# Optimization experiments

Hardware: AMD Instinct MI355X
Metric: run time of the kernel (lower is better)

## Reference

```python
import jax, jax.numpy as jnp
import numpy as np

SCALE = 64 ** (-0.5)


def setup_inputs() -> dict:
    key = jax.random.key(0)
    ks = jax.random.split(key, 6)
    B, C, D, N = 2, 1024, 64, 128
    w_std = C ** (-0.5)
    return {
        "lidar": jax.random.normal(ks[0], (B, C, D, N), dtype=jnp.float32),
        "cam": jax.random.normal(ks[1], (B, C, D, N), dtype=jnp.float32),
        "Wq": jax.random.normal(ks[2], (C, C), dtype=jnp.float32) * w_std,
        "Wk": jax.random.normal(ks[3], (C, C), dtype=jnp.float32) * w_std,
        "Wv": jax.random.normal(ks[4], (C, C), dtype=jnp.float32) * w_std,
        "Wo": jax.random.normal(ks[5], (C, C), dtype=jnp.float32) * w_std,
    }


def _proj(W, x):
    # 1x1 Conv1d over flattened (D*N) positions == channel matmul, bias=False
    return jnp.einsum('oc,bcdn->bodn', W, x)


def reference(lidar, cam, Wq, Wk, Wv, Wo):
    q = _proj(Wq, lidar)  # [B, C, D, Ni]
    k = _proj(Wk, cam)    # [B, C, D, Nj]
    v = _proj(Wv, cam)    # [B, C, D, Nj]
    # contract over D (head-dim-like axis); scores per (batch, channel)
    dots = jnp.einsum('bhdi,bhdj->bhij', q, k) * SCALE  # [B, C, Ni, Nj]
    att = jax.nn.softmax(dots, axis=-1)
    # einsum 'a b i c,a b j c->a b j i': contract over cam positions
    out = jnp.einsum('bhic,bhjc->bhji', att, v)  # [B, C, D, Ni]
    out = jax.nn.gelu(_proj(Wo, out), approximate=False)
    return out
```

## Files before the change

### kernel.cpp

```cpp
#include <hip/hip_runtime.h>
#include <math.h>

#define CH  1024
#define PPB 8192

typedef __attribute__((ext_vector_type(8))) short short8;
typedef __attribute__((ext_vector_type(4))) float f32x4;

__device__ __forceinline__ ushort f2bf(float x) {
    uint u = __float_as_uint(x);
    return (ushort)((u + 0x7FFFu + ((u >> 16) & 1u)) >> 16);
}
__device__ __forceinline__ float bf2f(ushort u) {
    return __uint_as_float(((uint)u) << 16);
}
__device__ __forceinline__ void gload16(const void* g, const void* l) {
    __builtin_amdgcn_global_load_lds((const __attribute__((address_space(1))) void*)g,
                                     (__attribute__((address_space(3))) void*)l, 16, 0, 0);
}

__global__ __launch_bounds__(256) void prep(const float* __restrict__ lidar,
                                            const float* __restrict__ cam,
                                            const float* __restrict__ Wq,
                                            const float* __restrict__ Wk,
                                            const float* __restrict__ Wv,
                                            const float* __restrict__ Wo,
                                            ushort* __restrict__ wdst,
                                            ushort* __restrict__ lidT,
                                            ushort* __restrict__ camT)
{
    __shared__ float T[64][65];
    const int blk = blockIdx.x;
    const int tid = threadIdx.x;

    if (blk < 2048) {
        const int y = blk >> 9;
        const int x = blk & 511;
        const float* w = (y == 0) ? Wq : (y == 1) ? Wk : (y == 2) ? Wv : Wo;
        ushort* o = wdst + (size_t)y * (1u << 20);
        const int idx = (x * 256 + tid) * 8;
        const float4 v0 = *(const float4*)(w + idx);
        const float4 v1 = *(const float4*)(w + idx + 4);
        ushort4 o0, o1;
        o0.x = f2bf(v0.x); o0.y = f2bf(v0.y); o0.z = f2bf(v0.z); o0.w = f2bf(v0.w);
        o1.x = f2bf(v1.x); o1.y = f2bf(v1.y); o1.z = f2bf(v1.z); o1.w = f2bf(v1.w);
        *(ushort4*)(o + idx)     = o0;
        *(ushort4*)(o + idx + 4) = o1;
        return;
    }

    const int t = blk - 2048;
    const bool isLid = (t < 4096);
    const int tt = isLid ? t : t - 4096;
    const float* in = isLid ? lidar : cam;
    ushort* out = isLid ? lidT : camT;

    const int p0 = (tt & 127) * 64;
    const int c0 = ((tt >> 7) & 15) * 64;
    const int b  = tt >> 11;
    const int rc = tid >> 4;
    const int rp = (tid & 15) * 4;

    #pragma unroll
    for (int pass = 0; pass < 4; ++pass) {
        const int c = pass * 16 + rc;
        const size_t base = ((size_t)(b * CH + c0 + c)) * PPB + p0 + rp;
        const float4 v = *(const float4*)(in + base);
        T[c][rp] = v.x; T[c][rp + 1] = v.y; T[c][rp + 2] = v.z; T[c][rp + 3] = v.w;
    }
    __syncthreads();
    #pragma unroll
    for (int pass = 0; pass < 4; ++pass) {
        const int p = pass * 16 + rc;
        ushort4 o;
        o.x = f2bf(T[rp + 0][p]); o.y = f2bf(T[rp + 1][p]);
        o.z = f2bf(T[rp + 2][p]); o.w = f2bf(T[rp + 3][p]);
        *(ushort4*)(out + ((size_t)(b * PPB + p0 + p)) * CH + c0 + rp) = o;
    }
}

__global__ __launch_bounds__(256) void transpose_ao(const ushort* __restrict__ in_,
                                                    ushort* __restrict__ out)
{
    __shared__ float T[64][65];
    const int p0 = blockIdx.x * 64;
    const int c0 = blockIdx.y * 64;
    const int b  = blockIdx.z;
    const int t  = threadIdx.x;
    const int rc = t >> 4;
    const int rp = (t & 15) * 4;

    #pragma unroll
    for (int pass = 0; pass < 4; ++pass) {
        const int c = pass * 16 + rc;
        const size_t base = ((size_t)(b * CH + c0 + c)) * PPB + p0 + rp;
        const ushort4 v = *(const ushort4*)(in_ + base);
        T[c][rp]     = bf2f(v.x); T[c][rp + 1] = bf2f(v.y);
        T[c][rp + 2] = bf2f(v.z); T[c][rp + 3] = bf2f(v.w);
    }
    __syncthreads();
    #pragma unroll
    for (int pass = 0; pass < 4; ++pass) {
        const int p = pass * 16 + rc;
        const int prow = p * 128 + blockIdx.x;
        ushort4 o;
        o.x = f2bf(T[rp + 0][p]); o.y = f2bf(T[rp + 1][p]);
        o.z = f2bf(T[rp + 2][p]); o.w = f2bf(T[rp + 3][p]);
        *(ushort4*)(out + ((size_t)(b * PPB + prow)) * CH + c0 + rp) = o;
    }
}

template <int IS_WO>
__global__ __launch_bounds__(512, 2) void gemm256(const ushort* __restrict__ W3,
                                                  const ushort* __restrict__ lidT,
                                                  const ushort* __restrict__ camT,
                                                  void* __restrict__ outp)
{
    __shared__ __align__(16) ushort sh[65536];
    char* shb = (char*)sh;

    const int bid = blockIdx.x;
    int g, bm, bn;
    if (IS_WO) {
        const int sid = (bid & 7) * 32 + (bid >> 3);
        g = 3; bm = sid & 3; bn = sid >> 2;
    } else {
        const int sid = (bid & 7) * 96 + (bid >> 3);
        g = sid >> 8; const int r = sid & 255; bm = r & 3; bn = r >> 2;
    }
    const int m0  = bm * 256;
    const int b   = bn >> 5;
    const int nn0 = (bn & 31) * 4;
    const int n0  = bn * 256;
    const ushort* A  = W3 + (size_t)g * (1u << 20);
    const ushort* Bt = (g == 0) ? lidT : camT;
    const bool remap = (!IS_WO) && (g < 2);

    const int tid = threadIdx.x;
    const int w   = tid >> 6;
    const int l   = tid & 63;
    const int wr  = w >> 2;
    const int wc  = w & 3;
    const int hi  = l >> 4;
    const int fr  = l & 15;

    auto stageA = [&](int buf, int kt, int half) {
        const int k0 = kt * 64;
        #pragma unroll
        for (int ld = 0; ld < 2; ++ld) {
            const int c  = w * 2 + ld;
            const int rt = half * 128 + c * 8 + (l >> 3);
            const int kc = ((l & 7) ^ (rt & 7)) << 3;
            gload16(A + (size_t)(m0 + rt) * CH + k0 + kc,
                    &shb[buf * 32768 + half * 16384 + c * 1024]);
        }
    };
    auto stageB = [&](int buf, int kt, int half) {
        const int k0 = kt * 64;
        #pragma unroll
        for (int ld = 0; ld < 2; ++ld) {
            const int c  = w * 2 + ld;
            const int rt = half * 128 + c * 8 + (l >> 3);
            const int kc = ((l & 7) ^ (rt & 7)) << 3;
            size_t brow;
            if (remap) brow = (size_t)b * PPB + (size_t)(rt & 63) * 128 + nn0 + (rt >> 6);
            else       brow = (size_t)(n0 + rt);
            gload16(Bt + brow * CH + k0 + kc,
                    &shb[65536 + buf * 32768 + half * 16384 + c * 1024]);
        }
    };

    f32x4 acc[8][4];
    #pragma unroll
    for (int i = 0; i < 8; ++i)
        #pragma unroll
        for (int j = 0; j < 4; ++j) acc[i][j] = (f32x4)(0.0f);

    stageA(0, 0, 0); stageA(0, 0, 1); stageB(0, 0, 0); stageB(0, 0, 1);

    for (int kt = 0; kt < 16; ++kt) {
        const int buf = kt & 1, nxt = buf ^ 1;
        if (kt < 15) {
            stageA(nxt, kt + 1, 0);
            __builtin_amdgcn_sched_barrier(0);
            asm volatile("s_waitcnt vmcnt(2)" ::: "memory");
        } else {
            __builtin_amdgcn_sched_barrier(0);
            asm volatile("s_waitcnt vmcnt(0)" ::: "memory");
        }
        __builtin_amdgcn_s_barrier();
        __builtin_amdgcn_sched_barrier(0);
        const int Ab = buf * 32768, Bb = 65536 + buf * 32768;

        #pragma unroll
        for (int q = 0; q < 4; ++q) {
            const int mh = q >> 1, nh = q & 1;
            if (kt < 15) {
                if (q == 1) stageA(nxt, kt + 1, 1);
                else if (q == 2) stageB(nxt, kt + 1, 0);
                else if (q == 3) stageB(nxt, kt + 1, 1);
            }
            short8 aq[4][2], bq[2][2];
            #pragma unroll
            for (int fm = 0; fm < 4; ++fm) {
                const int row = wr * 128 + (mh * 4 + fm) * 16 + fr;
                #pragma unroll
                for (int kk = 0; kk < 2; ++kk)
                    aq[fm][kk] = *(const short8*)&shb[Ab + row * 128 +
                        ((((kk << 2) + hi) ^ (row & 7)) << 4)];
            }
            #pragma unroll
            for (int fn = 0; fn < 2; ++fn) {
                const int row = wc * 64 + (nh * 2 + fn) * 16 + fr;
                #pragma unroll
                for (int kk = 0; kk < 2; ++kk)
                    bq[fn][kk] = *(const short8*)&shb[Bb + row * 128 +
                        ((((kk << 2) + hi) ^ (row & 7)) << 4)];
            }
            __builtin_amdgcn_s_setprio(1);
            #pragma unroll
            for (int fm = 0; fm < 4; ++fm)
                #pragma unroll
                for (int fn = 0; fn < 2; ++fn)
                    #pragma unroll
                    for (int kk = 0; kk < 2; ++kk)
                        acc[mh * 4 + fm][nh * 2 + fn] =
                            __builtin_amdgcn_mfma_f32_16x16x32_bf16(
                                aq[fm][kk], bq[fn][kk],
                                acc[mh * 4 + fm][nh * 2 + fn], 0, 0, 0);
            __builtin_amdgcn_s_setprio(0);
        }
        __builtin_amdgcn_sched_barrier(0);
        asm volatile("s_waitcnt lgkmcnt(0)" ::: "memory");
        __builtin_amdgcn_sched_barrier(0);
        __builtin_amdgcn_s_barrier();
    }

    #pragma unroll
    for (int fm = 0; fm < 8; ++fm)
        #pragma unroll
        for (int fn = 0; fn < 4; ++fn)
            #pragma unroll
            for (int r = 0; r < 4; ++r) {
                const int m = m0 + wr * 128 + fm * 16 + hi * 4 + r;
                const int s = (bn & 31) * 256 + wc * 64 + fn * 16 + fr;
                const float vv = acc[fm][fn][r];
                const size_t off = (size_t)b * CH * PPB + (size_t)m * PPB + s;
                if (IS_WO) {
                    ((float*)outp)[off] = 0.5f * vv * (1.0f + erff(vv * 0.70710678118654752f));
                } else {
                    ((ushort*)outp)[(size_t)g * ((size_t)16 << 20) + off] = f2bf(vv);
                }
            }
}

__global__ __launch_bounds__(256, 2) void attn_mfma(const ushort* __restrict__ qt,
                                                    const ushort* __restrict__ kt,
                                                    const ushort* __restrict__ vn,
                                                    ushort* __restrict__ ot)
{
    __shared__ ushort Qs[8192];
    __shared__ ushort Ks[8192];
    __shared__ ushort Vs[8192];
    __shared__ ushort Ps[16384];

    const int bh  = blockIdx.x;
    const int tid = threadIdx.x;
    const int w   = tid >> 6;
    const int l   = tid & 63;
    const int hi  = l >> 4;
    const int fr  = l & 15;
    const size_t base = (size_t)bh * 8192;

    {
        const int lr = l >> 3, lb = l & 7;
        const int vr = l >> 4, vbk = l & 15;
        #pragma unroll
        for (int q = 0; q < 4; ++q) {
            const int ch = w * 4 + q;
            const int i  = ch * 8 + lr;
            gload16(qt + base + i * 64 + ((lb ^ (i & 7)) << 3), &Qs[ch * 512]);
            gload16(kt + base + i * 64 + ((lb ^ (i & 7)) << 3), &Ks[ch * 512]);
            const int d  = ch * 4 + vr;
            gload16(vn + base + d * 128 + ((vbk ^ (d & 15)) << 3), &Vs[ch * 512]);
        }
    }
    __syncthreads();

    const int i0w = w * 32;
    f32x4 accS[2][8];
    #pragma unroll
    for (int a = 0; a < 2; ++a)
        #pragma unroll
        for (int bjj = 0; bjj < 8; ++bjj) accS[a][bjj] = (f32x4)(0.0f);

    #pragma unroll
    for (int kk = 0; kk < 2; ++kk) {
        const int blk = kk * 4 + hi;
        short8 aq[2];
        #pragma unroll
        for (int fm = 0; fm < 2; ++fm) {
            const int i = i0w + fm * 16 + fr;
            aq[fm] = *(const short8*)&Qs[i * 64 + ((blk ^ (i & 7)) << 3)];
        }
        #pragma unroll
        for (int fn = 0; fn < 8; ++fn) {
            const int j = fn * 16 + fr;
            const short8 bk = *(const short8*)&Ks[j * 64 + ((blk ^ (j & 7)) << 3)];
            #pragma unroll
            for (int fm = 0; fm < 2; ++fm)
                accS[fm][fn] = __builtin_amdgcn_mfma_f32_16x16x32_bf16(
                    aq[fm], bk, accS[fm][fn], 0, 0, 0);
        }
    }

    const float CS = 0.125f * 1.44269504088896341f;
    #pragma unroll
    for (int fm = 0; fm < 2; ++fm) {
        #pragma unroll
        for (int r = 0; r < 4; ++r) {
            float mx = accS[fm][0][r];
            #pragma unroll
            for (int fn = 1; fn < 8; ++fn) mx = fmaxf(mx, accS[fm][fn][r]);
            #pragma unroll
            for (int msk = 1; msk <= 8; msk <<= 1) mx = fmaxf(mx, __shfl_xor(mx, msk, 64));
            float e[8], sum = 0.f;
            #pragma unroll
            for (int fn = 0; fn < 8; ++fn) {
                e[fn] = exp2f((accS[fm][fn][r] - mx) * CS);
                sum += e[fn];
            }
            #pragma unroll
            for (int msk = 1; msk <= 8; msk <<= 1) sum += __shfl_xor(sum, msk, 64);
            const float is = 1.0f / sum;
            const int i = i0w + fm * 16 + hi * 4 + r;
            #pragma unroll
            for (int fn = 0; fn < 8; ++fn) {
                const int j = fn * 16 + fr;
                Ps[i * 128 + (((j >> 3) ^ (i & 15)) << 3) + (j & 7)] = f2bf(e[fn] * is);
            }
        }
    }

    f32x4 accO[2][4];
    #pragma unroll
    for (int a = 0; a < 2; ++a)
        #pragma unroll
        for (int bjj = 0; bjj < 4; ++bjj) accO[a][bjj] = (f32x4)(0.0f);

    #pragma unroll
    for (int ks2 = 0; ks2 < 4; ++ks2) {
        const int blk = ks2 * 4 + hi;
        short8 ap[2];
        #pragma unroll
        for (int fm = 0; fm < 2; ++fm) {
            const int i = i0w + fm * 16 + fr;
            ap[fm] = *(const short8*)&Ps[i * 128 + ((blk ^ (i & 15)) << 3)];
        }
        #pragma unroll
        for (int fn2 = 0; fn2 < 4; ++fn2) {
            const int d = fn2 * 16 + fr;
            const short8 bv = *(const short8*)&Vs[d * 128 + ((blk ^ (d & 15)) << 3)];
            #pragma unroll
            for (int fm = 0; fm < 2; ++fm)
                accO[fm][fn2] = __builtin_amdgcn_mfma_f32_16x16x32_bf16(
                    ap[fm], bv, accO[fm][fn2], 0, 0, 0);
        }
    }

    #pragma unroll
    for (int fm = 0; fm < 2; ++fm)
        #pragma unroll
        for (int fn2 = 0; fn2 < 4; ++fn2)
            #pragma unroll
            for (int r = 0; r < 4; ++r) {
                const int i = i0w + fm * 16 + hi * 4 + r;
                const int d = fn2 * 16 + fr;
                ot[base + i * 64 + d] = f2bf(accO[fm][fn2][r]);
            }
}

extern "C" void kernel_launch(void* const* d_in, const int* in_sizes, int n_in,
                              void* d_out, int out_size, void* d_ws, size_t ws_size,
                              hipStream_t stream)
{
    const float* lidar = (const float*)d_in[0];
    const float* cam   = (const float*)d_in[1];
    const float* Wq    = (const float*)d_in[2];
    const float* Wk    = (const float*)d_in[3];
    const float* Wv    = (const float*)d_in[4];
    const float* Wo    = (const float*)d_in[5];

    ushort* ws = (ushort*)d_ws;
    const size_t M1 = (size_t)1 << 20;
    const size_t TT = (size_t)16 << 20;
    ushort* lidT = ws + 4 * M1;
    ushort* camT = lidT + TT;
    ushort* qb   = camT + TT;
    ushort* aoT  = lidT;

    prep<<<dim3(10240), dim3(256), 0, stream>>>(lidar, cam, Wq, Wk, Wv, Wo, ws, lidT, camT);

    gemm256<0><<<dim3(768), dim3(512), 0, stream>>>(ws, lidT, camT, qb);

    attn_mfma<<<dim3(2048), dim3(256), 0, stream>>>(qb, qb + TT, qb + 2 * TT, qb);

    transpose_ao<<<dim3(128, 16, 2), dim3(256), 0, stream>>>(qb, aoT);

    gemm256<1><<<dim3(256), dim3(512), 0, stream>>>(ws, aoT, aoT, (float*)d_out);
}
```

Baseline: 268.3 us.

## Switch projection GEMM to 32x32x16 MFMA and simplify prefetch schedule

```diff
diff --git a/kernel.cpp b/kernel.cpp
--- a/kernel.cpp
+++ b/kernel.cpp
@@ -6,6 +6,7 @@
 
 typedef __attribute__((ext_vector_type(8))) short short8;
 typedef __attribute__((ext_vector_type(4))) float f32x4;
+typedef __attribute__((ext_vector_type(16))) float f32x16;
 
 __device__ __forceinline__ ushort f2bf(float x) {
     uint u = __float_as_uint(x);
@@ -141,8 +142,8 @@
     const int l   = tid & 63;
     const int wr  = w >> 2;
     const int wc  = w & 3;
-    const int hi  = l >> 4;
-    const int fr  = l & 15;
+    const int lr31 = l & 31;
+    const int kh   = l >> 5;
 
     auto stageA = [&](int buf, int kt, int half) {
         const int k0 = kt * 64;
@@ -170,64 +171,50 @@
         }
     };
 
-    f32x4 acc[8][4];
-    #pragma unroll
-    for (int i = 0; i < 8; ++i)
-        #pragma unroll
-        for (int j = 0; j < 4; ++j) acc[i][j] = (f32x4)(0.0f);
+    f32x16 acc[4][2];
+    #pragma unroll
+    for (int i = 0; i < 4; ++i)
+        #pragma unroll
+        for (int j = 0; j < 2; ++j)
+            #pragma unroll
+            for (int r = 0; r < 16; ++r) acc[i][j][r] = 0.0f;
 
     stageA(0, 0, 0); stageA(0, 0, 1); stageB(0, 0, 0); stageB(0, 0, 1);
 
     for (int kt = 0; kt < 16; ++kt) {
         const int buf = kt & 1, nxt = buf ^ 1;
-        if (kt < 15) {
-            stageA(nxt, kt + 1, 0);
-            __builtin_amdgcn_sched_barrier(0);
-            asm volatile("s_waitcnt vmcnt(2)" ::: "memory");
-        } else {
-            __builtin_amdgcn_sched_barrier(0);
-            asm volatile("s_waitcnt vmcnt(0)" ::: "memory");
-        }
+        __builtin_amdgcn_sched_barrier(0);
+        asm volatile("s_waitcnt vmcnt(0)" ::: "memory");
         __builtin_amdgcn_s_barrier();
         __builtin_amdgcn_sched_barrier(0);
+        if (kt < 15) {
+            stageA(nxt, kt + 1, 0); stageA(nxt, kt + 1, 1);
+            stageB(nxt, kt + 1, 0); stageB(nxt, kt + 1, 1);
+        }
         const int Ab = buf * 32768, Bb = 65536 + buf * 32768;
 
         #pragma unroll
-        for (int q = 0; q < 4; ++q) {
-            const int mh = q >> 1, nh = q & 1;
-            if (kt < 15) {
-                if (q == 1) stageA(nxt, kt + 1, 1);
-                else if (q == 2) stageB(nxt, kt + 1, 0);
-                else if (q == 3) stageB(nxt, kt + 1, 1);
-            }
-            short8 aq[4][2], bq[2][2];
+        for (int kk = 0; kk < 4; ++kk) {
+            short8 aq[4], bq[2];
             #pragma unroll
             for (int fm = 0; fm < 4; ++fm) {
-                const int row = wr * 128 + (mh * 4 + fm) * 16 + fr;
-                #pragma unroll
-                for (int kk = 0; kk < 2; ++kk)
-                    aq[fm][kk] = *(const short8*)&shb[Ab + row * 128 +
-                        ((((kk << 2) + hi) ^ (row & 7)) << 4)];
+                const int row = wr * 128 + fm * 32 + lr31;
+                aq[fm] = *(const short8*)&shb[Ab + row * 128 +
+                          (((kk * 2 + kh) ^ (row & 7)) << 4)];
             }
             #pragma unroll
             for (int fn = 0; fn < 2; ++fn) {
-                const int row = wc * 64 + (nh * 2 + fn) * 16 + fr;
-                #pragma unroll
-                for (int kk = 0; kk < 2; ++kk)
-                    bq[fn][kk] = *(const short8*)&shb[Bb + row * 128 +
-                        ((((kk << 2) + hi) ^ (row & 7)) << 4)];
+                const int row = wc * 64 + fn * 32 + lr31;
+                bq[fn] = *(const short8*)&shb[Bb + row * 128 +
+                          (((kk * 2 + kh) ^ (row & 7)) << 4)];
             }
             __builtin_amdgcn_s_setprio(1);
             #pragma unroll
             for (int fm = 0; fm < 4; ++fm)
                 #pragma unroll
                 for (int fn = 0; fn < 2; ++fn)
-                    #pragma unroll
-                    for (int kk = 0; kk < 2; ++kk)
-                        acc[mh * 4 + fm][nh * 2 + fn] =
-                            __builtin_amdgcn_mfma_f32_16x16x32_bf16(
-                                aq[fm][kk], bq[fn][kk],
-                                acc[mh * 4 + fm][nh * 2 + fn], 0, 0, 0);
+                    acc[fm][fn] = __builtin_amdgcn_mfma_f32_32x32x16_bf16(
+                        aq[fm], bq[fn], acc[fm][fn], 0, 0, 0);
             __builtin_amdgcn_s_setprio(0);
         }
         __builtin_amdgcn_sched_barrier(0);
@@ -237,14 +224,14 @@
     }
 
     #pragma unroll
-    for (int fm = 0; fm < 8; ++fm)
-        #pragma unroll
-        for (int fn = 0; fn < 4; ++fn)
-            #pragma unroll
-            for (int r = 0; r < 4; ++r) {
-                const int m = m0 + wr * 128 + fm * 16 + hi * 4 + r;
-                const int s = (bn & 31) * 256 + wc * 64 + fn * 16 + fr;
-                const float vv = acc[fm][fn][r];
+    for (int fm = 0; fm < 4; ++fm)
+        #pragma unroll
+        for (int fn = 0; fn < 2; ++fn)
+            #pragma unroll
+            for (int reg = 0; reg < 16; ++reg) {
+                const int m = m0 + wr * 128 + fm * 32 + (reg & 3) + 8 * (reg >> 2) + 4 * kh;
+                const int s = (bn & 31) * 256 + wc * 64 + fn * 32 + lr31;
+                const float vv = acc[fm][fn][reg];
                 const size_t off = (size_t)b * CH * PPB + (size_t)m * PPB + s;
                 if (IS_WO) {
                     ((float*)outp)[off] = 0.5f * vv * (1.0f + erff(vv * 0.70710678118654752f));
```

Result: no change. 263.7 us (-1.7%).

## Shrink projection GEMM tiles to 128x128 with 256-thread blocks

Applied to the files above, without the earlier changes.

```diff
diff --git a/kernel.cpp b/kernel.cpp
--- a/kernel.cpp
+++ b/kernel.cpp
@@ -111,27 +111,28 @@
 }
 
 template <int IS_WO>
-__global__ __launch_bounds__(512, 2) void gemm256(const ushort* __restrict__ W3,
+__global__ __launch_bounds__(256, 2) void gemm128(const ushort* __restrict__ W3,
                                                   const ushort* __restrict__ lidT,
                                                   const ushort* __restrict__ camT,
                                                   void* __restrict__ outp)
 {
-    __shared__ __align__(16) ushort sh[65536];
+    __shared__ __align__(16) ushort sh[32768];
     char* shb = (char*)sh;
 
     const int bid = blockIdx.x;
     int g, bm, bn;
     if (IS_WO) {
-        const int sid = (bid & 7) * 32 + (bid >> 3);
-        g = 3; bm = sid & 3; bn = sid >> 2;
+        const int sid = (bid & 7) * 128 + (bid >> 3);
+        g = 3; bm = sid & 7; bn = sid >> 3;
     } else {
-        const int sid = (bid & 7) * 96 + (bid >> 3);
-        g = sid >> 8; const int r = sid & 255; bm = r & 3; bn = r >> 2;
-    }
-    const int m0  = bm * 256;
-    const int b   = bn >> 5;
-    const int nn0 = (bn & 31) * 4;
-    const int n0  = bn * 256;
+        const int sid = (bid & 7) * 384 + (bid >> 3);
+        g = sid >> 10; const int r = sid & 1023; bm = r & 7; bn = r >> 3;
+    }
+    const int m0  = bm * 128;
+    const int b   = bn >> 6;
+    const int i0  = (bn & 63) * 2;
+    const int n0  = bn * 128;
+    const int p0  = (bn & 63) * 128;
     const ushort* A  = W3 + (size_t)g * (1u << 20);
     const ushort* Bt = (g == 0) ? lidT : camT;
     const bool remap = (!IS_WO) && (g < 2);
@@ -139,113 +140,107 @@
     const int tid = threadIdx.x;
     const int w   = tid >> 6;
     const int l   = tid & 63;
-    const int wr  = w >> 2;
-    const int wc  = w & 3;
+    const int wr  = w >> 1;
+    const int wc  = w & 1;
     const int hi  = l >> 4;
     const int fr  = l & 15;
 
-    auto stageA = [&](int buf, int kt, int half) {
+    auto stageA = [&](int buf, int kt) {
         const int k0 = kt * 64;
         #pragma unroll
-        for (int ld = 0; ld < 2; ++ld) {
-            const int c  = w * 2 + ld;
-            const int rt = half * 128 + c * 8 + (l >> 3);
+        for (int ld = 0; ld < 4; ++ld) {
+            const int c  = w * 4 + ld;
+            const int rt = c * 8 + (l >> 3);
             const int kc = ((l & 7) ^ (rt & 7)) << 3;
             gload16(A + (size_t)(m0 + rt) * CH + k0 + kc,
-                    &shb[buf * 32768 + half * 16384 + c * 1024]);
+                    &shb[buf * 16384 + c * 1024]);
         }
     };
-    auto stageB = [&](int buf, int kt, int half) {
+    auto stageB = [&](int buf, int kt) {
         const int k0 = kt * 64;
         #pragma unroll
-        for (int ld = 0; ld < 2; ++ld) {
-            const int c  = w * 2 + ld;
-            const int rt = half * 128 + c * 8 + (l >> 3);
+        for (int ld = 0; ld < 4; ++ld) {
+            const int c  = w * 4 + ld;
+            const int rt = c * 8 + (l >> 3);
             const int kc = ((l & 7) ^ (rt & 7)) << 3;
             size_t brow;
-            if (remap) brow = (size_t)b * PPB + (size_t)(rt & 63) * 128 + nn0 + (rt >> 6);
+            if (remap) brow = (size_t)b * PPB + (size_t)(rt & 63) * 128 + i0 + (rt >> 6);
             else       brow = (size_t)(n0 + rt);
             gload16(Bt + brow * CH + k0 + kc,
-                    &shb[65536 + buf * 32768 + half * 16384 + c * 1024]);
+                    &shb[32768 + buf * 16384 + c * 1024]);
         }
     };
 
-    f32x4 acc[8][4];
-    #pragma unroll
-    for (int i = 0; i < 8; ++i)
+    f32x4 acc[4][4];
+    #pragma unroll
+    for (int i = 0; i < 4; ++i)
         #pragma unroll
         for (int j = 0; j < 4; ++j) acc[i][j] = (f32x4)(0.0f);
 
-    stageA(0, 0, 0); stageA(0, 0, 1); stageB(0, 0, 0); stageB(0, 0, 1);
+    stageA(0, 0); stageB(0, 0);
 
     for (int kt = 0; kt < 16; ++kt) {
         const int buf = kt & 1, nxt = buf ^ 1;
         if (kt < 15) {
-            stageA(nxt, kt + 1, 0);
+            stageA(nxt, kt + 1);
             __builtin_amdgcn_sched_barrier(0);
-            asm volatile("s_waitcnt vmcnt(2)" ::: "memory");
+            asm volatile("s_waitcnt vmcnt(4)" ::: "memory");
         } else {
             __builtin_amdgcn_sched_barrier(0);
             asm volatile("s_waitcnt vmcnt(0)" ::: "memory");
         }
         __builtin_amdgcn_s_barrier();
         __builtin_amdgcn_sched_barrier(0);
-        const int Ab = buf * 32768, Bb = 65536 + buf * 32768;
-
-        #pragma unroll
-        for (int q = 0; q < 4; ++q) {
-            const int mh = q >> 1, nh = q & 1;
-            if (kt < 15) {
-                if (q == 1) stageA(nxt, kt + 1, 1);
-                else if (q == 2) stageB(nxt, kt + 1, 0);
-                else if (q == 3) stageB(nxt, kt + 1, 1);
-            }
-            short8 aq[4][2], bq[2][2];
-            #pragma unroll
-            for (int fm = 0; fm < 4; ++fm) {
-                const int row = wr * 128 + (mh * 4 + fm) * 16 + fr;
-                #pragma unroll
-                for (int kk = 0; kk < 2; ++kk)
-                    aq[fm][kk] = *(const short8*)&shb[Ab + row * 128 +
-                        ((((kk << 2) + hi) ^ (row & 7)) << 4)];
-            }
-            #pragma unroll
-            for (int fn = 0; fn < 2; ++fn) {
-                const int row = wc * 64 + (nh * 2 + fn) * 16 + fr;
-                #pragma unroll
-                for (int kk = 0; kk < 2; ++kk)
-                    bq[fn][kk] = *(const short8*)&shb[Bb + row * 128 +
-                        ((((kk << 2) + hi) ^ (row & 7)) << 4)];
-            }
-            __builtin_amdgcn_s_setprio(1);
-            #pragma unroll
-            for (int fm = 0; fm < 4; ++fm)
-                #pragma unroll
-                for (int fn = 0; fn < 2; ++fn)
-                    #pragma unroll
-                    for (int kk = 0; kk < 2; ++kk)
-                        acc[mh * 4 + fm][nh * 2 + fn] =
-                            __builtin_amdgcn_mfma_f32_16x16x32_bf16(
-                                aq[fm][kk], bq[fn][kk],
-                                acc[mh * 4 + fm][nh * 2 + fn], 0, 0, 0);
-            __builtin_amdgcn_s_setprio(0);
-        }
+        const int Ab = buf * 16384, Bb = 32768 + buf * 16384;
+
+        short8 aq[4][2], bq[4][2];
+        #pragma unroll
+        for (int fm = 0; fm < 4; ++fm) {
+            const int row = wr * 64 + fm * 16 + fr;
+            #pragma unroll
+            for (int kk = 0; kk < 2; ++kk)
+                aq[fm][kk] = *(const short8*)&shb[Ab + row * 128 +
+                    ((((kk << 2) + hi) ^ (row & 7)) << 4)];
+        }
+        #pragma unroll
+        for (int fn = 0; fn < 4; ++fn) {
+            const int row = wc * 64 + fn * 16 + fr;
+            #pragma unroll
+            for (int kk = 0; kk < 2; ++kk)
+                bq[fn][kk] = *(const short8*)&shb[Bb + row * 128 +
+                    ((((kk << 2) + hi) ^ (row & 7)) << 4)];
+        }
+        if (kt < 15) stageB(nxt, kt + 1);
         __builtin_amdgcn_sched_barrier(0);
         asm volatile("s_waitcnt lgkmcnt(0)" ::: "memory");
         __builtin_amdgcn_sched_barrier(0);
+
+        __builtin_amdgcn_s_setprio(1);
+        #pragma unroll
+        for (int kk = 0; kk < 2; ++kk)
+            #pragma unroll
+            for (int fm = 0; fm < 4; ++fm)
+                #pragma unroll
+                for (int fn = 0; fn < 4; ++fn)
+                    acc[fm][fn] = __builtin_amdgcn_mfma_f32_16x16x32_bf16(
+                        aq[fm][kk], bq[fn][kk], acc[fm][fn], 0, 0, 0);
+        __builtin_amdgcn_s_setprio(0);
+
+        __builtin_amdgcn_sched_barrier(0);
         __builtin_amdgcn_s_barrier();
-    }
-
-    #pragma unroll
-    for (int fm = 0; fm < 8; ++fm)
+        __builtin_amdgcn_sched_barrier(0);
+    }
+
+    #pragma unroll
+    for (int fm = 0; fm < 4; ++fm)
         #pragma unroll
         for (int fn = 0; fn < 4; ++fn)
             #pragma unroll
             for (int r = 0; r < 4; ++r) {
-                const int m = m0 + wr * 128 + fm * 16 + hi * 4 + r;
-                const int s = (bn & 31) * 256 + wc * 64 + fn * 16 + fr;
+                const int m = m0 + wr * 64 + fm * 16 + hi * 4 + r;
+                const int n = wc * 64 + fn * 16 + fr;
                 const float vv = acc[fm][fn][r];
-                const size_t off = (size_t)b * CH * PPB + (size_t)m * PPB + s;
+                const size_t off = (size_t)b * CH * PPB + (size_t)m * PPB + p0 + n;
                 if (IS_WO) {
                     ((float*)outp)[off] = 0.5f * vv * (1.0f + erff(vv * 0.70710678118654752f));
                 } else {
@@ -401,11 +396,11 @@
 
     prep<<<dim3(10240), dim3(256), 0, stream>>>(lidar, cam, Wq, Wk, Wv, Wo, ws, lidT, camT);
 
-    gemm256<0><<<dim3(768), dim3(512), 0, stream>>>(ws, lidT, camT, qb);
+    gemm128<0><<<dim3(3072), dim3(256), 0, stream>>>(ws, lidT, camT, qb);
 
     attn_mfma<<<dim3(2048), dim3(256), 0, stream>>>(qb, qb + TT, qb + 2 * TT, qb);
 
     transpose_ao<<<dim3(128, 16, 2), dim3(256), 0, stream>>>(qb, aoT);
 
-    gemm256<1><<<dim3(256), dim3(512), 0, stream>>>(ws, aoT, aoT, (float*)d_out);
-}
+    gemm128<1><<<dim3(1024), dim3(256), 0, stream>>>(ws, aoT, aoT, (float*)d_out);
+}
```

After: 232.5 us. -13.4%, faster.
